# Performance work log

Hardware: AMD Instinct MI355X
Metric: run time of the kernel (lower is better)

The kernel has to match this reference:

```python
import jax, jax.numpy as jnp
import numpy as np

N, D, H, DFF, NH = 8192, 128, 256, 2048, 2
HD = D // NH
DEG = 32
E = N * DEG
LN_EPS = 1e-5


def setup_inputs() -> dict:
    key = jax.random.key(0)
    ks = jax.random.split(key, 20)
    s = 0.02
    return {
        "x": jax.random.normal(ks[0], (N, D), jnp.float32),
        "edge_index": jax.random.randint(ks[1], (2, E), 0, N, jnp.int64),
        "beta": jnp.ones((), jnp.float32),  # AGNNConv learnable beta, init 1
        "in_proj_w": jax.random.normal(ks[2], (3 * D, D), jnp.float32) * s,
        "in_proj_b": jnp.zeros((3 * D,), jnp.float32),
        "out_proj_w": jax.random.normal(ks[3], (D, D), jnp.float32) * s,
        "out_proj_b": jnp.zeros((D,), jnp.float32),
        "ln1_g": jnp.ones((D,), jnp.float32),
        "ln1_b": jnp.zeros((D,), jnp.float32),
        "ff1_w": jax.random.normal(ks[4], (DFF, D), jnp.float32) * s,
        "ff1_b": jnp.zeros((DFF,), jnp.float32),
        "ff2_w": jax.random.normal(ks[5], (D, DFF), jnp.float32) * s,
        "ff2_b": jnp.zeros((D,), jnp.float32),
        "ln2_g": jnp.ones((D,), jnp.float32),
        "ln2_b": jnp.zeros((D,), jnp.float32),
        "fc_w": jax.random.normal(ks[6], (H, D), jnp.float32) * s,
        "fc_b": jnp.zeros((H,), jnp.float32),
        "head_w": jax.random.normal(ks[7], (2, H), jnp.float32) * s,
        "head_b": jnp.zeros((2,), jnp.float32),
    }


def _layernorm(x, g, b):
    mu = jnp.mean(x, axis=-1, keepdims=True)
    var = jnp.mean((x - mu) ** 2, axis=-1, keepdims=True)
    return (x - mu) * jax.lax.rsqrt(var + LN_EPS) * g + b


def _agnn(x, edge_index, beta):
    # PyG AGNNConv: add self-loops, cosine-sim attention, segment softmax over targets
    n = x.shape[0]
    loop = jnp.arange(n, dtype=edge_index.dtype)
    src = jnp.concatenate([edge_index[0], loop])  # message source j
    dst = jnp.concatenate([edge_index[1], loop])  # aggregation target i
    xn = x / jnp.maximum(jnp.linalg.norm(x, axis=-1, keepdims=True), 1e-12)
    alpha = beta * jnp.sum(xn[dst] * xn[src], axis=-1)  # [E+N]
    m = jax.ops.segment_max(alpha, dst, num_segments=n)
    e = jnp.exp(alpha - m[dst])
    z = jax.ops.segment_sum(e, dst, num_segments=n)
    w = e / z[dst]
    return jax.ops.segment_sum(w[:, None] * x[src], dst, num_segments=n)


def reference(x, edge_index, beta, in_proj_w, in_proj_b, out_proj_w, out_proj_b,
              ln1_g, ln1_b, ff1_w, ff1_b, ff2_w, ff2_b, ln2_g, ln2_b,
              fc_w, fc_b, head_w, head_b):
    h = _agnn(x, edge_index, beta)  # [N, D]
    # transformer sees shape [N, 1, D] with batch_first=False -> seq over all N nodes
    qkv = h @ in_proj_w.T + in_proj_b  # [N, 3D]
    q, k, v = jnp.split(qkv, 3, axis=-1)
    q = q.reshape(N, NH, HD).transpose(1, 0, 2)  # [h, N, hd]
    k = k.reshape(N, NH, HD).transpose(1, 0, 2)
    v = v.reshape(N, NH, HD).transpose(1, 0, 2)
    scores = jnp.einsum('hnd,hmd->hnm', q, k) / jnp.sqrt(jnp.float32(HD))
    attn = jax.nn.softmax(scores, axis=-1)
    o = jnp.einsum('hnm,hmd->hnd', attn, v).transpose(1, 0, 2).reshape(N, D)
    o = o @ out_proj_w.T + out_proj_b
    h = _layernorm(h + o, ln1_g, ln1_b)  # post-LN (norm_first=False)
    ff = jax.nn.relu(h @ ff1_w.T + ff1_b) @ ff2_w.T + ff2_b
    h = _layernorm(h + ff, ln2_g, ln2_b)
    h = jax.nn.relu(h @ fc_w.T + fc_b)
    return h @ head_w.T + head_b  # [N, 2]
```

## Files before the change

kernel.cpp:

```cpp
#include <hip/hip_runtime.h>


typedef __attribute__((ext_vector_type(4))) float  f32x4;
typedef __attribute__((ext_vector_type(8))) __bf16 bf16x8;

#define DEV __device__ __forceinline__

DEV unsigned short f2bf_bits(float f) {
  union { float f; unsigned u; } v; v.f = f;
  unsigned r = v.u + 0x7FFFu + ((v.u >> 16) & 1u);
  return (unsigned short)(r >> 16);
}

DEV __bf16 f2bf(float f) {
  union { unsigned short s; __bf16 b; } o; o.s = f2bf_bits(f);
  return o.b;
}

DEV f32x4 mfma16(bf16x8 a, bf16x8 b, f32x4 c) {
  return __builtin_amdgcn_mfma_f32_16x16x32_bf16(a, b, c, 0, 0, 0);
}

DEV bf16x8 ones8() {
  union { unsigned short s[8]; bf16x8 v; } u;
#pragma unroll
  for (int i = 0; i < 8; i++) u.s[i] = 0x3F80;
  return u.v;
}

DEV void ub8(bf16x8 v, float* f) {
  union { bf16x8 v; unsigned short s[8]; } u; u.v = v;
#pragma unroll
  for (int i = 0; i < 8; i++) {
    union { unsigned u; float f; } w; w.u = (unsigned)u.s[i] << 16;
    f[i] = w.f;
  }
}

#define GLD16(gp, lp) __builtin_amdgcn_global_load_lds(                        \
    (const __attribute__((address_space(1))) void*)(gp),                       \
    (__attribute__((address_space(3))) void*)(lp), 16, 0, 0)


__global__ __launch_bounds__(256) void k_prep(
    const float* __restrict__ x, float* __restrict__ inv,
    int* __restrict__ counts, const float* __restrict__ s0,
    const float* __restrict__ s1, const float* __restrict__ s2,
    const float* __restrict__ s3, const float* __restrict__ s4, __bf16* d0,
    __bf16* d1, __bf16* d2, __bf16* d3, __bf16* d4) {
  const int n0 = 384 * 128, n1 = 128 * 128, n2 = 2048 * 128, n3 = 128 * 2048,
            n4 = 256 * 128;
  if (blockIdx.x < 2048) {
    int lane = threadIdx.x & 63, w = threadIdx.x >> 6;
    int row = blockIdx.x * 4 + w;
    float2 v = ((const float2*)(x + (size_t)row * 128))[lane];
    float s = v.x * v.x + v.y * v.y;
#pragma unroll
    for (int m = 1; m < 64; m <<= 1) s += __shfl_xor(s, m);
    if (lane == 0) {
      inv[row] = 1.f / fmaxf(sqrtf(s), 1e-12f);
      counts[row] = 0;
    }
    return;
  }
  int t = (blockIdx.x - 2048) * 256 + threadIdx.x;
  if (t < n0) { d0[t] = f2bf(s0[t]); return; } t -= n0;
  if (t < n1) { d1[t] = f2bf(s1[t]); return; } t -= n1;
  if (t < n2) { d2[t] = f2bf(s2[t]); return; } t -= n2;
  if (t < n3) { d3[t] = f2bf(s3[t]); return; } t -= n3;
  if (t < n4) { d4[t] = f2bf(s4[t]); }
}


__global__ void k_count(const int* __restrict__ ei, int* __restrict__ counts,
                        int E) {
  int e = blockIdx.x * 256 + threadIdx.x;
  if (e < E) atomicAdd(&counts[ei[E + e]], 1);
}

__global__ __launch_bounds__(256) void k_scan(const int* __restrict__ counts,
                                              int* __restrict__ offs,
                                              int* __restrict__ cursor) {
  __shared__ int sums[256];
  int t = threadIdx.x, base = t * 32;
  int s = 0;
  for (int i = 0; i < 32; i++) s += counts[base + i];
  sums[t] = s;
  __syncthreads();
  for (int off = 1; off < 256; off <<= 1) {
    int v = (t >= off) ? sums[t - off] : 0;
    __syncthreads();
    sums[t] += v;
    __syncthreads();
  }
  int run = sums[t] - s;
  for (int i = 0; i < 32; i++) {
    offs[base + i] = run; cursor[base + i] = run;
    run += counts[base + i];
  }
  if (t == 255) offs[8192] = run;
}

__global__ void k_scatter(const int* __restrict__ ei, int* __restrict__ cursor,
                          int* __restrict__ csr, int E) {
  int e = blockIdx.x * 256 + threadIdx.x;
  if (e < E) {
    int dst = ei[E + e];
    int pos = atomicAdd(&cursor[dst], 1);
    csr[pos] = ei[e];
  }
}

__global__ __launch_bounds__(256) void k_agnn(
    const float* __restrict__ x, const int* __restrict__ csr,
    const int* __restrict__ offs, const float* __restrict__ inv,
    const float* __restrict__ betap, float* __restrict__ hf,
    __bf16* __restrict__ hb) {
  int lane = threadIdx.x & 63, w = threadIdx.x >> 6;
  int dst = blockIdx.x * 4 + w;
  float beta = *betap;
  float2 xd = ((const float2*)(x + (size_t)dst * 128))[lane];
  float invd = inv[dst];
  float sd = xd.x * xd.x + xd.y * xd.y;
#pragma unroll
  for (int m = 1; m < 64; m <<= 1) sd += __shfl_xor(sd, m);
  float z = __expf(beta * sd * invd * invd);
  float ax = z * xd.x, ay = z * xd.y;
  int e0 = offs[dst], e1 = offs[dst + 1];
  int e = e0;
  for (; e + 2 <= e1; e += 2) {
    int s0 = csr[e], s1 = csr[e + 1];
    float2 xa = ((const float2*)(x + (size_t)s0 * 128))[lane];
    float2 xb = ((const float2*)(x + (size_t)s1 * 128))[lane];
    float ia = inv[s0], ib = inv[s1];
    float da = xd.x * xa.x + xd.y * xa.y;
    float db = xd.x * xb.x + xd.y * xb.y;
#pragma unroll
    for (int m = 1; m < 64; m <<= 1) {
      da += __shfl_xor(da, m);
      db += __shfl_xor(db, m);
    }
    float sa = __expf(beta * da * invd * ia);
    float sb = __expf(beta * db * invd * ib);
    z += sa + sb;
    ax += sa * xa.x + sb * xb.x;
    ay += sa * xa.y + sb * xb.y;
  }
  if (e < e1) {
    int s0 = csr[e];
    float2 xa = ((const float2*)(x + (size_t)s0 * 128))[lane];
    float da = xd.x * xa.x + xd.y * xa.y;
#pragma unroll
    for (int m = 1; m < 64; m <<= 1) da += __shfl_xor(da, m);
    float sa = __expf(beta * da * invd * inv[s0]);
    z += sa; ax += sa * xa.x; ay += sa * xa.y;
  }
  float r = 1.f / z;
  ax *= r; ay *= r;
  float2 o; o.x = ax; o.y = ay;
  ((float2*)(hf + (size_t)dst * 128))[lane] = o;
  hb[(size_t)dst * 128 + 2 * lane]     = f2bf(ax);
  hb[(size_t)dst * 128 + 2 * lane + 1] = f2bf(ay);
}

__global__ __launch_bounds__(256, 3) void k_gemm(
    const __bf16* __restrict__ A, const __bf16* __restrict__ B,
    const float* __restrict__ bias, float* __restrict__ Cf,
    __bf16* __restrict__ Cb, float* __restrict__ Cpart, int M, int N, int K,
    int relu) {
  __shared__ __bf16 As[128 * 64];
  __shared__ __bf16 Bs[128 * 64];
  const int tid = threadIdx.x, lane = tid & 63, wid = tid >> 6;
  const int wm = wid & 1, wn = wid >> 1;
  const int bm = blockIdx.x * 128, bn = blockIdx.y * 128;
  const int kz = blockIdx.z, nkz = gridDim.z;
  const int kchunk = K / nkz, k0beg = kz * kchunk, k0end = k0beg + kchunk;
  const int lr = lane >> 3, lc8 = (lane & 7) * 8;
  const int l15 = lane & 15, quad = lane >> 4, kq = quad * 8;

  f32x4 acc[4][4] = {};
  const __bf16* Ab = A + (size_t)(bm + lr) * K + lc8;
  const __bf16* Bb = B + (size_t)(bn + lr) * K + lc8;

  for (int k0 = k0beg; k0 < k0end; k0 += 64) {
#pragma unroll
    for (int i = 0; i < 4; i++) {
      int j = wid * 4 + i;
      GLD16(Ab + (size_t)(8 * j) * K + k0, &As[j * 512]);
      GLD16(Bb + (size_t)(8 * j) * K + k0, &Bs[j * 512]);
    }
    __syncthreads();
    const int ar = (wm * 64 + l15) * 64 + kq;
    const int br = (wn * 64 + l15) * 64 + kq;
#pragma unroll
    for (int kk = 0; kk < 2; kk++) {
      bf16x8 a[4], b[4];
#pragma unroll
      for (int mt = 0; mt < 4; mt++)
        a[mt] = *(const bf16x8*)&As[ar + mt * 1024 + kk * 32];
#pragma unroll
      for (int nt = 0; nt < 4; nt++)
        b[nt] = *(const bf16x8*)&Bs[br + nt * 1024 + kk * 32];
#pragma unroll
      for (int mt = 0; mt < 4; mt++)
#pragma unroll
        for (int nt = 0; nt < 4; nt++)
          acc[mt][nt] = mfma16(a[mt], b[nt], acc[mt][nt]);
    }
    __syncthreads();
  }
  const int col0 = bn + wn * 64 + l15;
  const int row0 = bm + wm * 64 + quad * 4;
  if (Cpart) {
    float* P = Cpart + (size_t)kz * M * N;
#pragma unroll
    for (int mt = 0; mt < 4; mt++)
#pragma unroll
      for (int nt = 0; nt < 4; nt++)
#pragma unroll
        for (int r = 0; r < 4; r++)
          P[(size_t)(row0 + mt * 16 + r) * N + col0 + nt * 16] = acc[mt][nt][r];
  } else {
#pragma unroll
    for (int nt = 0; nt < 4; nt++) {
      float bv = bias[col0 + nt * 16];
#pragma unroll
      for (int mt = 0; mt < 4; mt++)
#pragma unroll
        for (int r = 0; r < 4; r++) {
          float v = acc[mt][nt][r] + bv;
          if (relu) v = fmaxf(v, 0.f);
          size_t idx = (size_t)(row0 + mt * 16 + r) * N + col0 + nt * 16;
          if (Cf) Cf[idx] = v;
          if (Cb) Cb[idx] = f2bf(v);
        }
    }
  }
}

__global__ __launch_bounds__(256, 2) void k_gemm_qkv(
    const __bf16* __restrict__ A, const __bf16* __restrict__ B,
    const float* __restrict__ bias, __bf16* __restrict__ Qb,
    __bf16* __restrict__ Kb, __bf16* __restrict__ Vtb) {
  __shared__ __bf16 smem[17408];
  __bf16* As = smem;
  __bf16* Bs = smem + 8192;
  const int K = 128;
  const int tid = threadIdx.x, lane = tid & 63, wid = tid >> 6;
  const int wm = wid & 1, wn = wid >> 1;
  const int bm = blockIdx.x * 128, y = blockIdx.y, bn = y * 128;
  const int lr = lane >> 3, lc8 = (lane & 7) * 8;
  const int l15 = lane & 15, quad = lane >> 4, kq = quad * 8;
  const float qscale = 0.125f * 1.44269504089f;

  f32x4 acc[4][4] = {};
  const __bf16* Ab = A + (size_t)(bm + lr) * K + lc8;
  const __bf16* Bb = B + (size_t)(bn + lr) * K + lc8;

  for (int k0 = 0; k0 < 128; k0 += 64) {
#pragma unroll
    for (int i = 0; i < 4; i++) {
      int j = wid * 4 + i;
      GLD16(Ab + (size_t)(8 * j) * K + k0, &As[j * 512]);
      GLD16(Bb + (size_t)(8 * j) * K + k0, &Bs[j * 512]);
    }
    __syncthreads();
    const int ar = (wm * 64 + l15) * 64 + kq;
    const int br = (wn * 64 + l15) * 64 + kq;
#pragma unroll
    for (int kk = 0; kk < 2; kk++) {
      bf16x8 a[4], b[4];
#pragma unroll
      for (int mt = 0; mt < 4; mt++)
        a[mt] = *(const bf16x8*)&As[ar + mt * 1024 + kk * 32];
#pragma unroll
      for (int nt = 0; nt < 4; nt++)
        b[nt] = *(const bf16x8*)&Bs[br + nt * 1024 + kk * 32];
#pragma unroll
      for (int mt = 0; mt < 4; mt++)
#pragma unroll
        for (int nt = 0; nt < 4; nt++)
          acc[mt][nt] = mfma16(a[mt], b[nt], acc[mt][nt]);
    }
    __syncthreads();
  }

  if (y < 2) {
    __bf16* D = (y == 0) ? Qb : Kb;
    float sc = (y == 0) ? qscale : 1.f;
    int h = wn;
#pragma unroll
    for (int nt = 0; nt < 4; nt++) {
      int c = wn * 64 + nt * 16 + l15;
      float bv = bias[bn + c];
      int d = nt * 16 + l15;
#pragma unroll
      for (int mt = 0; mt < 4; mt++)
#pragma unroll
        for (int r = 0; r < 4; r++) {
          int row = bm + wm * 64 + mt * 16 + quad * 4 + r;
          D[(size_t)h * 524288 + (size_t)row * 64 + d] =
              f2bf((acc[mt][nt][r] + bv) * sc);
        }
    }
  } else {
#pragma unroll
    for (int nt = 0; nt < 4; nt++) {
      int c = wn * 64 + nt * 16 + l15;
      float bv = bias[bn + c];
#pragma unroll
      for (int mt = 0; mt < 4; mt++)
#pragma unroll
        for (int r = 0; r < 4; r++) {
          int nl = wm * 64 + mt * 16 + quad * 4 + r;
          smem[nl * 136 + c] = f2bf(acc[mt][nt][r] + bv);
        }
    }
    __syncthreads();
    int d = tid >> 1, nh = tid & 1;
    __bf16* dst = Vtb + (size_t)d * 8192 + bm + nh * 64;
#pragma unroll
    for (int i = 0; i < 8; i++) {
      union { unsigned short s[8]; bf16x8 v; } u;
#pragma unroll
      for (int e = 0; e < 8; e++)
        u.s[e] = *(const unsigned short*)&smem[(nh * 64 + i * 8 + e) * 136 + d];
      *(bf16x8*)(dst + i * 8) = u.v;
    }
  }
}

__global__ __launch_bounds__(256, 2) void k_attn(
    const __bf16* __restrict__ Qb, const __bf16* __restrict__ Kb,
    const __bf16* __restrict__ Vtb, __bf16* __restrict__ Opart,
    float* __restrict__ Lpart) {
  __shared__ __bf16 Ks[4096];
  __shared__ __bf16 Vs[4096];
  __shared__ __bf16 Ps[4][64 * 72];

  const int tid = threadIdx.x, lane = tid & 63, w = tid >> 6;
  const int qt = blockIdx.x, h = blockIdx.y, kz = blockIdx.z;
  const int qbase = qt * 256;
  const int l15 = lane & 15, quad = lane >> 4;
  const int lofs = lane * 8;

  const __bf16* Qg = Qb + ((size_t)h * 8192 + qbase) * 64;
  const __bf16* Kg = Kb + (size_t)h * 8192 * 64;
  const __bf16* Vg = Vtb + (size_t)h * 64 * 8192;
  const bf16x8 vone = ones8();

  __bf16* Qstage = &Ps[0][0];
#pragma unroll
  for (int i = 0; i < 4; i++) {
    int j = w * 4 + i;
#pragma unroll
    for (int hh = 0; hh < 2; hh++)
      GLD16(Qg + (size_t)(j * 16 + l15) * 64 + hh * 32 + quad * 8,
            Qstage + j * 1024 + hh * 512);
  }
  __syncthreads();
  bf16x8 aq[4][2];
#pragma unroll
  for (int s = 0; s < 4; s++) {
    const __bf16* base = Qstage + (size_t)(w * 4 + s) * 1024;
    aq[s][0] = *(const bf16x8*)&base[lofs];
    aq[s][1] = *(const bf16x8*)&base[512 + lofs];
  }
  __syncthreads();

  f32x4 o[4][4] = {};
  f32x4 lacc[4] = {};
  const int kstart = kz * 1024;

  for (int kt = 0; kt < 16; kt++) {
    int kb = kstart + kt * 64;
#pragma unroll
    for (int hh = 0; hh < 2; hh++) {
      GLD16(Kg + (size_t)(kb + w * 16 + l15) * 64 + hh * 32 + quad * 8,
            &Ks[w * 1024 + hh * 512]);
      GLD16(Vg + (size_t)(w * 16 + l15) * 8192 + kb + hh * 32 + quad * 8,
            &Vs[w * 1024 + hh * 512]);
    }
    __syncthreads();

#pragma unroll
    for (int mt = 0; mt < 4; mt++) {
      bf16x8 k0 = *(const bf16x8*)&Ks[mt * 1024 + lofs];
      bf16x8 k1 = *(const bf16x8*)&Ks[mt * 1024 + 512 + lofs];
#pragma unroll
      for (int s = 0; s < 4; s++) {
        f32x4 St = {};
        St = mfma16(k0, aq[s][0], St);
        St = mfma16(k1, aq[s][1], St);
        union { float f; unsigned u; } p0, p1, p2, p3;
        p0.f = __builtin_amdgcn_exp2f(St[0]);
        p1.f = __builtin_amdgcn_exp2f(St[1]);
        p2.f = __builtin_amdgcn_exp2f(St[2]);
        p3.f = __builtin_amdgcn_exp2f(St[3]);
        uint2 pk;
        pk.x = (p0.u >> 16) | (p1.u & 0xFFFF0000u);
        pk.y = (p2.u >> 16) | (p3.u & 0xFFFF0000u);
        *(uint2*)&Ps[w][(s * 16 + l15) * 72 + mt * 16 + quad * 4] = pk;
      }
    }
    bf16x8 vf[4][2];
#pragma unroll
    for (int nd = 0; nd < 4; nd++) {
      vf[nd][0] = *(const bf16x8*)&Vs[nd * 1024 + lofs];
      vf[nd][1] = *(const bf16x8*)&Vs[nd * 1024 + 512 + lofs];
    }
#pragma unroll
    for (int s = 0; s < 4; s++) {
      bf16x8 ap0 = *(const bf16x8*)&Ps[w][(s * 16 + l15) * 72 + quad * 8];
      bf16x8 ap1 = *(const bf16x8*)&Ps[w][(s * 16 + l15) * 72 + 32 + quad * 8];
      lacc[s] = mfma16(ap0, vone, lacc[s]);
      lacc[s] = mfma16(ap1, vone, lacc[s]);
#pragma unroll
      for (int nd = 0; nd < 4; nd++) {
        o[s][nd] = mfma16(ap0, vf[nd][0], o[s][nd]);
        o[s][nd] = mfma16(ap1, vf[nd][1], o[s][nd]);
      }
    }
    __syncthreads();
  }

  const size_t bpart = (size_t)(h * 8 + kz);
#pragma unroll
  for (int s = 0; s < 4; s++) {
#pragma unroll
    for (int nd = 0; nd < 4; nd++)
#pragma unroll
      for (int r = 0; r < 4; r++) {
        int row = qbase + w * 64 + s * 16 + quad * 4 + r;
        Opart[(bpart * 8192 + row) * 64 + nd * 16 + l15] = f2bf(o[s][nd][r]);
      }
    if (l15 == 0) {
#pragma unroll
      for (int r = 0; r < 4; r++) {
        int row = qbase + w * 64 + s * 16 + quad * 4 + r;
        Lpart[bpart * 8192 + row] = lacc[s][r];
      }
    }
  }
}

__global__ __launch_bounds__(256) void k_oproj_ln(
    const __bf16* __restrict__ Opart, const float* __restrict__ Lpart,
    const __bf16* __restrict__ Wo, const float* __restrict__ ob,
    const float* __restrict__ hf, const float* __restrict__ g,
    const float* __restrict__ bt, float* __restrict__ h1f,
    __bf16* __restrict__ h1b) {
  __shared__ __bf16 Af[4 * 2048];
  __shared__ __bf16 Bf[8 * 2048];
  __shared__ float scr1[64][2], scr2[64][2];
  const int tid = threadIdx.x, lane = tid & 63, w = tid >> 6;
  const int l15 = lane & 15, quad = lane >> 4;
  const int lofs = lane * 8;
  const int bm = blockIdx.x * 64;
  const int wm = w & 1, wn = w >> 1;

#pragma unroll
  for (int f = 0; f < 2; f++) {
    int j = w * 2 + f;
#pragma unroll
    for (int kq = 0; kq < 4; kq++)
      GLD16(Wo + (size_t)(j * 16 + l15) * 128 + kq * 32 + quad * 8,
            &Bf[j * 2048 + kq * 512]);
  }
  {
    int n = bm + w * 16 + l15;
    float L0 = 0.f, L1 = 0.f;
#pragma unroll
    for (int z = 0; z < 8; z++) {
      L0 += Lpart[(size_t)z * 8192 + n];
      L1 += Lpart[(size_t)(8 + z) * 8192 + n];
    }
    float r0 = 1.f / L0, r1 = 1.f / L1;
#pragma unroll
    for (int kq = 0; kq < 4; kq++) {
      int hh = kq >> 1;
      int d0 = (kq & 1) * 32 + quad * 8;
      float acc8[8] = {};
#pragma unroll
      for (int z = 0; z < 8; z++) {
        bf16x8 t = *(const bf16x8*)&Opart[((size_t)(hh * 8 + z) * 8192 + n) *
                                              64 + d0];
        float f[8];
        ub8(t, f);
#pragma unroll
        for (int e = 0; e < 8; e++) acc8[e] += f[e];
      }
      float rh = hh ? r1 : r0;
      union { unsigned short s[8]; bf16x8 v; } u;
#pragma unroll
      for (int e = 0; e < 8; e++) u.s[e] = f2bf_bits(acc8[e] * rh);
      *(bf16x8*)&Af[w * 2048 + kq * 512 + lane * 8] = u.v;
    }
  }
  __syncthreads();

  f32x4 acc[2][4] = {};
#pragma unroll
  for (int kq = 0; kq < 4; kq++) {
    bf16x8 a[2], b[4];
#pragma unroll
    for (int mt = 0; mt < 2; mt++)
      a[mt] = *(const bf16x8*)&Af[(wm * 2 + mt) * 2048 + kq * 512 + lofs];
#pragma unroll
    for (int nt = 0; nt < 4; nt++)
      b[nt] = *(const bf16x8*)&Bf[(wn * 4 + nt) * 2048 + kq * 512 + lofs];
#pragma unroll
    for (int mt = 0; mt < 2; mt++)
#pragma unroll
      for (int nt = 0; nt < 4; nt++)
        acc[mt][nt] = mfma16(a[mt], b[nt], acc[mt][nt]);
  }

  float v[2][4][4];
#pragma unroll
  for (int mt = 0; mt < 2; mt++)
#pragma unroll
    for (int r = 0; r < 4; r++) {
      int row = bm + wm * 32 + mt * 16 + quad * 4 + r;
      float s1 = 0.f, s2 = 0.f;
#pragma unroll
      for (int nt = 0; nt < 4; nt++) {
        int col = wn * 64 + nt * 16 + l15;
        float val = acc[mt][nt][r] + ob[col] + hf[(size_t)row * 128 + col];
        v[mt][nt][r] = val;
        s1 += val;
        s2 += val * val;
      }
#pragma unroll
      for (int msk = 1; msk < 16; msk <<= 1) {
        s1 += __shfl_xor(s1, msk);
        s2 += __shfl_xor(s2, msk);
      }
      if (l15 == 0) {
        int rl = wm * 32 + mt * 16 + quad * 4 + r;
        scr1[rl][wn] = s1;
        scr2[rl][wn] = s2;
      }
    }
  __syncthreads();
#pragma unroll
  for (int mt = 0; mt < 2; mt++)
#pragma unroll
    for (int r = 0; r < 4; r++) {
      int rl = wm * 32 + mt * 16 + quad * 4 + r;
      int row = bm + rl;
      float S1 = scr1[rl][0] + scr1[rl][1];
      float S2 = scr2[rl][0] + scr2[rl][1];
      float mu = S1 * (1.f / 128.f);
      float var = S2 * (1.f / 128.f) - mu * mu;
      float rstd = rsqrtf(var + 1e-5f);
#pragma unroll
      for (int nt = 0; nt < 4; nt++) {
        int col = wn * 64 + nt * 16 + l15;
        float y = (v[mt][nt][r] - mu) * rstd * g[col] + bt[col];
        h1f[(size_t)row * 128 + col] = y;
        h1b[(size_t)row * 128 + col] = f2bf(y);
      }
    }
}

__global__ __launch_bounds__(256) void k_tail(
    const float* __restrict__ h1f, const float* __restrict__ part,
    const float* __restrict__ pbias, const float* __restrict__ g,
    const float* __restrict__ bt, const __bf16* __restrict__ Wfc,
    const float* __restrict__ fcb, const float* __restrict__ hw,
    const float* __restrict__ hb, float* __restrict__ out) {
  __shared__ __bf16 Af[2 * 2048];
  __shared__ __bf16 Bf[16 * 2048];
  __shared__ float scr0[32][4], scr1[32][4];
  const int tid = threadIdx.x, lane = tid & 63, w = tid >> 6;
  const int l15 = lane & 15, quad = lane >> 4;
  const int lofs = lane * 8;
  const int bm = blockIdx.x * 32;

  if (w >= 2) {
#pragma unroll
    for (int f = 0; f < 8; f++) {
      int j = (w - 2) * 8 + f;
#pragma unroll
      for (int kq = 0; kq < 4; kq++)
        GLD16(Wfc + (size_t)(j * 16 + l15) * 128 + kq * 32 + quad * 8,
              &Bf[j * 2048 + kq * 512]);
    }
  } else {
    int row = bm + w * 16 + l15;
    float val[4][8];
    float s1 = 0.f, s2 = 0.f;
#pragma unroll
    for (int kq = 0; kq < 4; kq++) {
      int c0 = kq * 32 + quad * 8;
      const float* h1p = h1f + (size_t)row * 128 + c0;
#pragma unroll
      for (int j = 0; j < 8; j++) val[kq][j] = h1p[j] + pbias[c0 + j];
#pragma unroll
      for (int z = 0; z < 8; z++) {
        const float* pp = part + (size_t)z * 1048576 + (size_t)row * 128 + c0;
#pragma unroll
        for (int j = 0; j < 8; j++) val[kq][j] += pp[j];
      }
#pragma unroll
      for (int j = 0; j < 8; j++) {
        s1 += val[kq][j];
        s2 += val[kq][j] * val[kq][j];
      }
    }
    s1 += __shfl_xor(s1, 16); s1 += __shfl_xor(s1, 32);
    s2 += __shfl_xor(s2, 16); s2 += __shfl_xor(s2, 32);
    float mu = s1 * (1.f / 128.f);
    float var = s2 * (1.f / 128.f) - mu * mu;
    float rstd = rsqrtf(var + 1e-5f);
#pragma unroll
    for (int kq = 0; kq < 4; kq++) {
      int c0 = kq * 32 + quad * 8;
      union { unsigned short s[8]; bf16x8 v; } u;
#pragma unroll
      for (int j = 0; j < 8; j++)
        u.s[j] = f2bf_bits((val[kq][j] - mu) * rstd * g[c0 + j] + bt[c0 + j]);
      *(bf16x8*)&Af[w * 2048 + kq * 512 + lane * 8] = u.v;
    }
  }
  __syncthreads();

  f32x4 acc[2][4] = {};
#pragma unroll
  for (int kq = 0; kq < 4; kq++) {
    bf16x8 a[2], b[4];
#pragma unroll
    for (int mt = 0; mt < 2; mt++)
      a[mt] = *(const bf16x8*)&Af[mt * 2048 + kq * 512 + lofs];
#pragma unroll
    for (int nt = 0; nt < 4; nt++)
      b[nt] = *(const bf16x8*)&Bf[(w * 4 + nt) * 2048 + kq * 512 + lofs];
#pragma unroll
    for (int mt = 0; mt < 2; mt++)
#pragma unroll
      for (int nt = 0; nt < 4; nt++)
        acc[mt][nt] = mfma16(a[mt], b[nt], acc[mt][nt]);
  }

#pragma unroll
  for (int mt = 0; mt < 2; mt++)
#pragma unroll
    for (int r = 0; r < 4; r++) {
      float p0 = 0.f, p1 = 0.f;
#pragma unroll
      for (int nt = 0; nt < 4; nt++) {
        int col = w * 64 + nt * 16 + l15;
        float vv = fmaxf(acc[mt][nt][r] + fcb[col], 0.f);
        p0 += vv * hw[col];
        p1 += vv * hw[256 + col];
      }
#pragma unroll
      for (int msk = 1; msk < 16; msk <<= 1) {
        p0 += __shfl_xor(p0, msk);
        p1 += __shfl_xor(p1, msk);
      }
      if (l15 == 0) {
        int rl = mt * 16 + quad * 4 + r;
        scr0[rl][w] = p0;
        scr1[rl][w] = p1;
      }
    }
  __syncthreads();
  if (tid < 32) {
    float p0 = scr0[tid][0] + scr0[tid][1] + scr0[tid][2] + scr0[tid][3];
    float p1 = scr1[tid][0] + scr1[tid][1] + scr1[tid][2] + scr1[tid][3];
    out[(size_t)(bm + tid) * 2]     = p0 + hb[0];
    out[(size_t)(bm + tid) * 2 + 1] = p1 + hb[1];
  }
}

extern "C" void kernel_launch(void* const* d_in, const int* in_sizes, int n_in,
                              void* d_out, int out_size, void* d_ws,
                              size_t ws_size, hipStream_t stream) {
  const float* x     = (const float*)d_in[0];
  const int*   ei    = (const int*)d_in[1];
  const float* beta  = (const float*)d_in[2];
  const float* in_w  = (const float*)d_in[3];
  const float* in_b  = (const float*)d_in[4];
  const float* out_w = (const float*)d_in[5];
  const float* out_b = (const float*)d_in[6];
  const float* ln1g  = (const float*)d_in[7];
  const float* ln1b  = (const float*)d_in[8];
  const float* ff1w  = (const float*)d_in[9];
  const float* ff1b  = (const float*)d_in[10];
  const float* ff2w  = (const float*)d_in[11];
  const float* ff2b  = (const float*)d_in[12];
  const float* ln2g  = (const float*)d_in[13];
  const float* ln2b  = (const float*)d_in[14];
  const float* fcw   = (const float*)d_in[15];
  const float* fcb   = (const float*)d_in[16];
  const float* hw    = (const float*)d_in[17];
  const float* hbias = (const float*)d_in[18];
  float* out = (float*)d_out;
  const int N = 8192;
  const int E = in_sizes[1] / 2;

  char* wsp = (char*)d_ws;
  size_t off = 0;
  auto alloc = [&](size_t b) -> void* {
    void* p = wsp + off;
    off = (off + b + 255) & ~(size_t)255;
    return p;
  };

  float*  inv     = (float*)alloc((size_t)N * 4);
  int*    counts  = (int*)alloc((size_t)N * 4);
  int*    offs    = (int*)alloc((size_t)(N + 1) * 4);
  int*    cursor  = (int*)alloc((size_t)N * 4);
  int*    csr     = (int*)alloc((size_t)E * 4);
  float*  h_f     = (float*)alloc((size_t)N * 128 * 4);
  __bf16* h_b     = (__bf16*)alloc((size_t)N * 128 * 2);
  float*  h1_f    = (float*)alloc((size_t)N * 128 * 4);
  __bf16* h1_b    = (__bf16*)alloc((size_t)N * 128 * 2);
  float*  Lpart   = (float*)alloc((size_t)16 * N * 4);
  __bf16* w_in    = (__bf16*)alloc((size_t)384 * 128 * 2);
  __bf16* w_out   = (__bf16*)alloc((size_t)128 * 128 * 2);
  __bf16* w_ff1   = (__bf16*)alloc((size_t)2048 * 128 * 2);
  __bf16* w_ff2   = (__bf16*)alloc((size_t)128 * 2048 * 2);
  __bf16* w_fc    = (__bf16*)alloc((size_t)256 * 128 * 2);
  char*   bigA    = (char*)alloc((size_t)16 * N * 64 * 4);
  __bf16* Opart   = (__bf16*)bigA;
  __bf16* ff1o    = (__bf16*)bigA;
  char*   bigB    = (char*)alloc((size_t)33554432);
  __bf16* Qb      = (__bf16*)bigB;
  __bf16* Kb      = (__bf16*)(bigB + 2097152);
  __bf16* Vtb     = (__bf16*)(bigB + 2 * 2097152);
  float*  ff2part = (float*)bigB;
  (void)ws_size; (void)n_in; (void)out_size;

  k_prep<<<4784, 256, 0, stream>>>(x, inv, counts, in_w, out_w, ff1w, ff2w,
                                   fcw, w_in, w_out, w_ff1, w_ff2, w_fc);
  k_count<<<(E + 255) / 256, 256, 0, stream>>>(ei, counts, E);
  k_scan<<<1, 256, 0, stream>>>(counts, offs, cursor);
  k_scatter<<<(E + 255) / 256, 256, 0, stream>>>(ei, cursor, csr, E);
  k_agnn<<<N / 4, 256, 0, stream>>>(x, csr, offs, inv, beta, h_f, h_b);

  k_gemm_qkv<<<dim3(64, 3), 256, 0, stream>>>(h_b, w_in, in_b, Qb, Kb, Vtb);
  k_attn<<<dim3(32, 2, 8), 256, 0, stream>>>(Qb, Kb, Vtb, Opart, Lpart);
  k_oproj_ln<<<128, 256, 0, stream>>>(Opart, Lpart, w_out, out_b, h_f, ln1g,
                                      ln1b, h1_f, h1_b);
  k_gemm<<<dim3(64, 16, 1), 256, 0, stream>>>(h1_b, w_ff1, ff1b, nullptr, ff1o,
                                              nullptr, N, 2048, 128, 1);
  k_gemm<<<dim3(64, 1, 8), 256, 0, stream>>>(ff1o, w_ff2, nullptr, nullptr,
                                             nullptr, ff2part, N, 128, 2048, 0);
  k_tail<<<256, 256, 0, stream>>>(h1_f, ff2part, ff2b, ln2g, ln2b, w_fc, fcb,
                                  hw, hbias, out);
}
```

Measured before the change: 261.9 us.

## Double-buffer K/V tiles in attention kernel to overlap loads with MFMA

The attention kernel now keeps two LDS buffers for each of K and V. It issues the global-to-LDS load for the next key tile right after the barrier, then computes on the current tile, so memory latency can overlap with the QK and PV MFMA work. The trailing barrier in each iteration is removed, leaving one barrier per tile. In exchange, LDS use per block goes up by 16 KB, which could limit occupancy, and correctness depends on the barrier also waiting for the outstanding async loads.

Result: no change. 263.3 us (+0.5%).

```diff
diff --git a/kernel.cpp b/kernel.cpp
--- a/kernel.cpp
+++ b/kernel.cpp
@@ -334,8 +334,8 @@
     const __bf16* __restrict__ Qb, const __bf16* __restrict__ Kb,
     const __bf16* __restrict__ Vtb, __bf16* __restrict__ Opart,
     float* __restrict__ Lpart) {
-  __shared__ __bf16 Ks[4096];
-  __shared__ __bf16 Vs[4096];
+  __shared__ __bf16 Ks[2][4096];
+  __shared__ __bf16 Vs[2][4096];
   __shared__ __bf16 Ps[4][64 * 72];
 
   const int tid = threadIdx.x, lane = tid & 63, w = tid >> 6;
@@ -372,21 +372,32 @@
   f32x4 lacc[4] = {};
   const int kstart = kz * 1024;
 
+#pragma unroll
+  for (int hh = 0; hh < 2; hh++) {
+    GLD16(Kg + (size_t)(kstart + w * 16 + l15) * 64 + hh * 32 + quad * 8,
+          &Ks[0][w * 1024 + hh * 512]);
+    GLD16(Vg + (size_t)(w * 16 + l15) * 8192 + kstart + hh * 32 + quad * 8,
+          &Vs[0][w * 1024 + hh * 512]);
+  }
+
   for (int kt = 0; kt < 16; kt++) {
-    int kb = kstart + kt * 64;
-#pragma unroll
-    for (int hh = 0; hh < 2; hh++) {
-      GLD16(Kg + (size_t)(kb + w * 16 + l15) * 64 + hh * 32 + quad * 8,
-            &Ks[w * 1024 + hh * 512]);
-      GLD16(Vg + (size_t)(w * 16 + l15) * 8192 + kb + hh * 32 + quad * 8,
-            &Vs[w * 1024 + hh * 512]);
-    }
+    const int cur = kt & 1;
     __syncthreads();
+    if (kt + 1 < 16) {
+      int kb2 = kstart + (kt + 1) * 64;
+#pragma unroll
+      for (int hh = 0; hh < 2; hh++) {
+        GLD16(Kg + (size_t)(kb2 + w * 16 + l15) * 64 + hh * 32 + quad * 8,
+              &Ks[cur ^ 1][w * 1024 + hh * 512]);
+        GLD16(Vg + (size_t)(w * 16 + l15) * 8192 + kb2 + hh * 32 + quad * 8,
+              &Vs[cur ^ 1][w * 1024 + hh * 512]);
+      }
+    }
 
 #pragma unroll
     for (int mt = 0; mt < 4; mt++) {
-      bf16x8 k0 = *(const bf16x8*)&Ks[mt * 1024 + lofs];
-      bf16x8 k1 = *(const bf16x8*)&Ks[mt * 1024 + 512 + lofs];
+      bf16x8 k0 = *(const bf16x8*)&Ks[cur][mt * 1024 + lofs];
+      bf16x8 k1 = *(const bf16x8*)&Ks[cur][mt * 1024 + 512 + lofs];
 #pragma unroll
       for (int s = 0; s < 4; s++) {
         f32x4 St = {};
@@ -406,8 +417,8 @@
     bf16x8 vf[4][2];
 #pragma unroll
     for (int nd = 0; nd < 4; nd++) {
-      vf[nd][0] = *(const bf16x8*)&Vs[nd * 1024 + lofs];
-      vf[nd][1] = *(const bf16x8*)&Vs[nd * 1024 + 512 + lofs];
+      vf[nd][0] = *(const bf16x8*)&Vs[cur][nd * 1024 + lofs];
+      vf[nd][1] = *(const bf16x8*)&Vs[cur][nd * 1024 + 512 + lofs];
     }
 #pragma unroll
     for (int s = 0; s < 4; s++) {
@@ -421,7 +432,6 @@
         o[s][nd] = mfma16(ap1, vf[nd][1], o[s][nd]);
       }
     }
-    __syncthreads();
   }
 
   const size_t bpart = (size_t)(h * 8 + kz);
```
